# Optimization experiments

Measured on AMD Instinct MI355X. Metric: run time of the kernel, lower is better.

The kernel has to match this reference:

```python
import math
import jax, jax.numpy as jnp
import numpy as np

NUM_BUCKETS = 32
MAX_DISTANCE = 128
N_HEADS = 16
D_KV = 64


def _relative_position_bucket(relative_position, num_buckets=NUM_BUCKETS, max_distance=MAX_DISTANCE):
    # bidirectional variant (encoder): half the buckets for each sign
    nb = num_buckets // 2
    n = -relative_position
    ret = (n < 0).astype(jnp.int32) * nb
    n = jnp.abs(n)
    max_exact = nb // 2
    is_small = n < max_exact
    val_if_large = max_exact + (
        jnp.log(jnp.maximum(n, 1).astype(jnp.float32) / max_exact)
        / math.log(max_distance / max_exact)
        * (nb - max_exact)
    ).astype(jnp.int32)
    val_if_large = jnp.minimum(val_if_large, nb - 1)
    return ret + jnp.where(is_small, n, val_if_large)


def setup_inputs() -> dict:
    key = jax.random.key(0)
    ks = jax.random.split(key, 6)
    d_model = 1024
    inner = N_HEADS * D_KV
    scale = 1.0 / math.sqrt(d_model)
    x = jax.random.normal(ks[0], (2, 2048, d_model), dtype=jnp.float32)
    wq = jax.random.normal(ks[1], (d_model, inner), dtype=jnp.float32) * scale
    wk = jax.random.normal(ks[2], (d_model, inner), dtype=jnp.float32) * scale
    wv = jax.random.normal(ks[3], (d_model, inner), dtype=jnp.float32) * scale
    wo = jax.random.normal(ks[4], (inner, d_model), dtype=jnp.float32) * scale
    rel_emb = jax.random.normal(ks[5], (NUM_BUCKETS, N_HEADS), dtype=jnp.float32)
    return {"x": x, "wq": wq, "wk": wk, "wv": wv, "wo": wo, "rel_emb": rel_emb}


def reference(x, wq, wk, wv, wo, rel_emb):
    B, S, D = x.shape
    # QKV projections (no bias, T5 style), split heads -> [B, S, H, Dk]
    q = (x @ wq).reshape(B, S, N_HEADS, D_KV)
    k = (x @ wk).reshape(B, S, N_HEADS, D_KV)
    v = (x @ wv).reshape(B, S, N_HEADS, D_KV)
    # NOTE: T5 does NOT scale by 1/sqrt(d_kv)
    scores = jnp.einsum("bqhd,bkhd->bhqk", q, k)  # [B, H, S, S]
    # relative position bias
    ctx = jnp.arange(S)[:, None]
    mem = jnp.arange(S)[None, :]
    buckets = _relative_position_bucket(mem - ctx)  # [S, S]
    bias = rel_emb[buckets]  # [S, S, H]
    bias = jnp.transpose(bias, (2, 0, 1))[None]  # [1, H, S, S]
    scores = scores + bias
    weights = jax.nn.softmax(scores.astype(jnp.float32), axis=-1).astype(scores.dtype)
    context = jnp.einsum("bhqk,bkhd->bqhd", weights, v).reshape(B, S, N_HEADS * D_KV)
    return context @ wo
```

## Files before the change

### kernel.cpp

```cpp
#include <hip/hip_runtime.h>
#include <hip/hip_bf16.h>

typedef __attribute__((ext_vector_type(8))) _Float16 f16x8;
typedef __attribute__((ext_vector_type(4))) float f32x4;
typedef unsigned short u16;
typedef unsigned int u32;

#define S_LEN 2048
#define NH    16
#define DK    64
#define DMODEL 1024
#define LOG2E 1.44269504f
#define NTILES (S_LEN / 64)

union F16U { _Float16 h; u16 u; };
__device__ __forceinline__ u16 f2h(float f) {
    F16U v; v.h = (_Float16)f; return v.u;
}

__device__ __forceinline__ void gl16(const u16* g, u16* l) {
    __builtin_amdgcn_global_load_lds(
        (__attribute__((address_space(1))) void*)(u16*)g,
        (__attribute__((address_space(3))) void*)l, 16, 0, 0);
}

__global__ __launch_bounds__(256) void prep_kernel(
    const float* __restrict__ X,
    const float* __restrict__ Wq, const float* __restrict__ Wk,
    const float* __restrict__ Wv, const float* __restrict__ Wo,
    const float* __restrict__ rel_emb,
    u16* __restrict__ Xf, u16* __restrict__ WT, float* __restrict__ tab)
{
    __shared__ __align__(16) float T[64 * 68];
    const int bid = blockIdx.x;
    const int tid = threadIdx.x;

    if (bid < 2048) {
        long i8 = ((long)bid * 256 + tid) * 8;
        float4 a = *(const float4*)&X[i8];
        float4 b = *(const float4*)&X[i8 + 4];
        *(ushort4*)&Xf[i8] =
            make_ushort4(f2h(a.x), f2h(a.y), f2h(a.z), f2h(a.w));
        *(ushort4*)&Xf[i8 + 4] =
            make_ushort4(f2h(b.x), f2h(b.y), f2h(b.z), f2h(b.w));
    } else if (bid < 3072) {
        const int w0 = bid - 2048;
        const int z = w0 >> 8, rem = w0 & 255;
        const int k0 = (rem >> 4) * 64, n0 = (rem & 15) * 64;
        const float* src = (z == 0) ? Wq : (z == 1) ? Wk
                         : (z == 2) ? Wv : Wo;
        u16* dT = WT + (long)z * 1048576;
        #pragma unroll
        for (int u = 0; u < 4; u++) {
            int w = tid + u * 256;
            int r = w >> 4, c4 = (w & 15) * 4;
            *(float4*)&T[r * 68 + c4] =
                *(const float4*)&src[(long)(k0 + r) * DMODEL + n0 + c4];
        }
        __syncthreads();
        #pragma unroll
        for (int u = 0; u < 4; u++) {
            int w = tid + u * 256;
            int n = w >> 4, kc = (w & 15) * 4;
            *(ushort4*)&dT[(long)(n0 + n) * DMODEL + k0 + kc] = make_ushort4(
                f2h(T[(kc + 0) * 68 + n]), f2h(T[(kc + 1) * 68 + n]),
                f2h(T[(kc + 2) * 68 + n]), f2h(T[(kc + 3) * 68 + n]));
        }
    } else {
        int idx = (bid - 3072) * 256 + tid;
        int h = idx >> 12;
        int t = idx & 4095;
        int rp = t - 2048;
        int n = -rp;
        int ret = 0;
        if (n < 0) { ret = 16; n = -n; }
        int inner;
        if (n < 8) {
            inner = n;
        } else {
            inner = 8 + (n >= 12) + (n >= 16) + (n >= 23) + (n >= 32)
                      + (n >= 46) + (n >= 64) + (n >= 91);
            if (inner > 15) inner = 15;
        }
        tab[h * 4096 + t] = rel_emb[(ret + inner) * NH + h] * LOG2E;
    }
}

__global__ __launch_bounds__(256, 3) void gemm_qkv_mfma(
    const u16* __restrict__ Xf, const u16* __restrict__ WT,
    u16* __restrict__ Qf, u16* __restrict__ Kf, u16* __restrict__ VT)
{
    const int z = blockIdx.z;
    const u16* BT = WT + (long)z * 1048576;

    __shared__ __align__(16) u16 Ah[128 * 64], Bh[128 * 64];

    const int tid = threadIdx.x;
    const int wv = tid >> 6, lane = tid & 63;
    const int g = lane >> 4, li = lane & 15;
    const int wr = wv >> 1, wc = wv & 1;
    const int bm = blockIdx.y * 128, bn = blockIdx.x * 128;

    const int sr = lane >> 3;
    const int sb = ((lane & 7) ^ sr) * 8;
    const u16* Asrc[4]; const u16* Bsrc[4];
    u16* Adst[4]; u16* Bdst[4];
    #pragma unroll
    for (int u = 0; u < 4; u++) {
        const int c = wv * 4 + u;
        const int row = c * 8 + sr;
        Asrc[u] = &Xf[(long)(bm + row) * DMODEL + sb];
        Bsrc[u] = &BT[(long)(bn + row) * DMODEL + sb];
        Adst[u] = &Ah[c * 512];
        Bdst[u] = &Bh[c * 512];
    }

    int roA[4][2], roB[4][2];
    #pragma unroll
    for (int i = 0; i < 4; i++)
        #pragma unroll
        for (int ks = 0; ks < 2; ks++) {
            int RA = wr * 64 + i * 16 + li;
            int RB = wc * 64 + i * 16 + li;
            roA[i][ks] = RA * 64 + (((ks * 4 + g) ^ (li & 7)) * 8);
            roB[i][ks] = RB * 64 + (((ks * 4 + g) ^ (li & 7)) * 8);
        }

    f32x4 acc[4][4];
    #pragma unroll
    for (int i = 0; i < 4; i++)
        #pragma unroll
        for (int j = 0; j < 4; j++) acc[i][j] = (f32x4){0.f, 0.f, 0.f, 0.f};

    for (int k0 = 0; k0 < DMODEL; k0 += 64) {
        #pragma unroll
        for (int u = 0; u < 4; u++) {
            gl16(Asrc[u] + k0, Adst[u]);
            gl16(Bsrc[u] + k0, Bdst[u]);
        }
        __syncthreads();

        #pragma unroll
        for (int ks = 0; ks < 2; ks++) {
            f16x8 a_h[4], b_h[4];
            #pragma unroll
            for (int i = 0; i < 4; i++) a_h[i] = *(const f16x8*)&Ah[roA[i][ks]];
            #pragma unroll
            for (int j = 0; j < 4; j++) b_h[j] = *(const f16x8*)&Bh[roB[j][ks]];
            #pragma unroll
            for (int i = 0; i < 4; i++)
                #pragma unroll
                for (int j = 0; j < 4; j++)
                    acc[i][j] = __builtin_amdgcn_mfma_f32_16x16x32_f16(
                        a_h[i], b_h[j], acc[i][j], 0, 0, 0);
        }
        __syncthreads();
    }

    if (z == 2) {
        #pragma unroll
        for (int i = 0; i < 4; i++) {
            int s_base = bm + wr * 64 + i * 16 + g * 4;
            int bb = s_base >> 11, s = s_base & 2047;
            #pragma unroll
            for (int j = 0; j < 4; j++) {
                int gcol = bn + wc * 64 + j * 16 + li;
                int hh = gcol >> 6, d = gcol & 63;
                long idx = (((long)(bb * NH + hh)) * DK + d) * S_LEN + s;
                *(ushort4*)&VT[idx] = make_ushort4(
                    f2h(acc[i][j][0]), f2h(acc[i][j][1]),
                    f2h(acc[i][j][2]), f2h(acc[i][j][3]));
            }
        }
    } else {
        u16* O = (z == 0) ? Qf : Kf;
        #pragma unroll
        for (int i = 0; i < 4; i++) {
            #pragma unroll
            for (int r = 0; r < 4; r++) {
                int grow = bm + wr * 64 + i * 16 + g * 4 + r;
                int bb = grow >> 11, s = grow & 2047;
                #pragma unroll
                for (int j = 0; j < 4; j++) {
                    int gcol = bn + wc * 64 + j * 16 + li;
                    int hh = gcol >> 6, d = gcol & 63;
                    long idx = (((long)(bb * NH + hh)) * S_LEN + s) * DK + d;
                    O[idx] = f2h(acc[i][j][r]);
                }
            }
        }
    }
}

__global__ __launch_bounds__(256, 3) void gemm_out_mfma(
    const u16* __restrict__ Ab, const u16* __restrict__ WT,
    float* __restrict__ O)
{
    const u16* BT = WT + 3L * 1048576;
    __shared__ __align__(16) u16 Ah[128 * 64], Bh[128 * 64];

    const int tid = threadIdx.x;
    const int wv = tid >> 6, lane = tid & 63;
    const int g = lane >> 4, li = lane & 15;
    const int wr = wv >> 1, wc = wv & 1;
    const int bm = blockIdx.y * 128, bn = blockIdx.x * 128;

    const int sr = lane >> 3;
    const int sb = ((lane & 7) ^ sr) * 8;
    const u16* Asrc[4]; const u16* Bsrc[4];
    u16* Adst[4]; u16* Bdst[4];
    #pragma unroll
    for (int u = 0; u < 4; u++) {
        const int c = wv * 4 + u;
        const int row = c * 8 + sr;
        Asrc[u] = &Ab[(long)(bm + row) * DMODEL + sb];
        Bsrc[u] = &BT[(long)(bn + row) * DMODEL + sb];
        Adst[u] = &Ah[c * 512];
        Bdst[u] = &Bh[c * 512];
    }

    int roA[4][2], roB[4][2];
    #pragma unroll
    for (int i = 0; i < 4; i++)
        #pragma unroll
        for (int ks = 0; ks < 2; ks++) {
            int RA = wr * 64 + i * 16 + li;
            int RB = wc * 64 + i * 16 + li;
            roA[i][ks] = RA * 64 + (((ks * 4 + g) ^ (li & 7)) * 8);
            roB[i][ks] = RB * 64 + (((ks * 4 + g) ^ (li & 7)) * 8);
        }

    f32x4 acc[4][4];
    #pragma unroll
    for (int i = 0; i < 4; i++)
        #pragma unroll
        for (int j = 0; j < 4; j++) acc[i][j] = (f32x4){0.f, 0.f, 0.f, 0.f};

    for (int k0 = 0; k0 < DMODEL; k0 += 64) {
        #pragma unroll
        for (int u = 0; u < 4; u++) {
            gl16(Asrc[u] + k0, Adst[u]);
            gl16(Bsrc[u] + k0, Bdst[u]);
        }
        __syncthreads();

        #pragma unroll
        for (int ks = 0; ks < 2; ks++) {
            f16x8 a_h[4], b_h[4];
            #pragma unroll
            for (int i = 0; i < 4; i++) a_h[i] = *(const f16x8*)&Ah[roA[i][ks]];
            #pragma unroll
            for (int j = 0; j < 4; j++) b_h[j] = *(const f16x8*)&Bh[roB[j][ks]];
            #pragma unroll
            for (int i = 0; i < 4; i++)
                #pragma unroll
                for (int j = 0; j < 4; j++)
                    acc[i][j] = __builtin_amdgcn_mfma_f32_16x16x32_f16(
                        a_h[i], b_h[j], acc[i][j], 0, 0, 0);
        }
        __syncthreads();
    }

    #pragma unroll
    for (int i = 0; i < 4; i++)
        #pragma unroll
        for (int r = 0; r < 4; r++) {
            int grow = bm + wr * 64 + i * 16 + g * 4 + r;
            #pragma unroll
            for (int j = 0; j < 4; j++) {
                int gcol = bn + wc * 64 + j * 16 + li;
                O[(long)grow * DMODEL + gcol] = acc[i][j][r];
            }
        }
}

__global__ __launch_bounds__(256, 4) void attn_mfma(
    const u16* __restrict__ Qf, const u16* __restrict__ Kf,
    const u16* __restrict__ VT, const float* __restrict__ tab,
    u16* __restrict__ ctxb)
{
    __shared__ __align__(16) u16 Ks[2][4096];
    __shared__ __align__(16) u16 Vs[2][4096];

    const int tid = threadIdx.x;
    const int wv = tid >> 6, lane = tid & 63;
    const int g = lane >> 4, li = lane & 15;

    const int nbid = (blockIdx.x & 7) * 128 + (blockIdx.x >> 3);
    const int qblk = nbid & 31;
    const int h = (nbid >> 5) & 15;
    const int b = nbid >> 9;
    const int q0 = qblk * 64;
    const long bh = b * NH + h;
    const int qloc = wv * 16 + li;

    const u16* KhG = Kf + bh * (S_LEN * DK);
    const u16* VtG = VT + bh * (DK * S_LEN);
    const float* th0 = tab + h * 4096;
    const float* thq = th0 + 2048 - q0 - qloc + g * 4;

    const int sr  = lane >> 3;
    const int sd8 = ((lane & 7) ^ sr) * 8;
    const int c0 = wv * 2, c1 = wv * 2 + 1;
    const u16* Kg0 = KhG + (long)(c0 * 8 + sr) * DK + sd8;
    const u16* Kg1 = KhG + (long)(c1 * 8 + sr) * DK + sd8;
    const u16* Vg0 = VtG + (long)(c0 * 8 + sr) * S_LEN + sd8;
    const u16* Vg1 = VtG + (long)(c1 * 8 + sr) * S_LEN + sd8;

    const int sw  = (li & 7) * 8;
    const int roA = (g * 8) ^ sw;
    const int roB = (g * 8 + 32) ^ sw;
    const int rrow = li * 64;

    f16x8 q0f, q1f;
    {
        long qrow = bh * S_LEN + q0 + qloc;
        const u16* ph = Qf + qrow * DK + g * 8;
        q0f = *(const f16x8*)ph;  q1f = *(const f16x8*)(ph + 32);
    }
    const float bias_hi = th0[2048 + 512];
    const float bias_lo = th0[2048 - 512];

    gl16(Kg0, &Ks[0][c0 * 512]);
    gl16(Kg1, &Ks[0][c1 * 512]);
    gl16(Vg0, &Vs[0][c0 * 512]);
    gl16(Vg1, &Vs[0][c1 * 512]);
    __syncthreads();

    f32x4 Oc[4];
    #pragma unroll
    for (int n = 0; n < 4; n++) Oc[n] = (f32x4){0.f, 0.f, 0.f, 0.f};
    float mP = -1e30f, lR = 0.f;

    int cur = 0;
    for (int t = 0; t < NTILES; ++t) {
        const int kt0 = t * 64;

        if (t + 1 < NTILES) {
            const long ko = (long)(kt0 + 64) * DK;
            gl16(Kg0 + ko, &Ks[cur ^ 1][c0 * 512]);
            gl16(Kg1 + ko, &Ks[cur ^ 1][c1 * 512]);
            gl16(Vg0 + kt0 + 64, &Vs[cur ^ 1][c0 * 512]);
            gl16(Vg1 + kt0 + 64, &Vs[cur ^ 1][c1 * 512]);
        }

        float bia[4][4];
        const int dd = kt0 - q0;
        if (dd >= 192 || dd <= -192) {
            const float bc = (dd > 0) ? bias_hi : bias_lo;
            #pragma unroll
            for (int m = 0; m < 4; m++)
                #pragma unroll
                for (int r = 0; r < 4; r++) bia[m][r] = bc;
        } else {
            const float* tb = thq + kt0;
            #pragma unroll
            for (int m = 0; m < 4; m++)
                #pragma unroll
                for (int r = 0; r < 4; r++) bia[m][r] = tb[m * 16 + r];
        }

        f32x4 Sa[4];
        __builtin_amdgcn_s_setprio(1);
        #pragma unroll
        for (int m = 0; m < 4; m++) {
            const u16* kp = &Ks[cur][m * 1024 + rrow];
            f16x8 k0 = *(const f16x8*)(kp + roA);
            f16x8 k1 = *(const f16x8*)(kp + roB);
            f32x4 s = (f32x4){0.f, 0.f, 0.f, 0.f};
            s = __builtin_amdgcn_mfma_f32_16x16x32_f16(k0, q0f, s, 0, 0, 0);
            s = __builtin_amdgcn_mfma_f32_16x16x32_f16(k1, q1f, s, 0, 0, 0);
            Sa[m] = s;
        }
        __builtin_amdgcn_s_setprio(0);

        #pragma unroll
        for (int m = 0; m < 4; m++)
            #pragma unroll
            for (int r = 0; r < 4; r++)
                Sa[m][r] = fmaf(Sa[m][r], LOG2E, bia[m][r]);

        float mm[4];
        #pragma unroll
        for (int m = 0; m < 4; m++)
            mm[m] = fmaxf(fmaxf(Sa[m][0], Sa[m][1]),
                          fmaxf(Sa[m][2], Sa[m][3]));
        float pm = fmaxf(fmaxf(mm[0], mm[1]), fmaxf(mm[2], mm[3]));
        pm = fmaxf(pm, __shfl_xor(pm, 16));
        pm = fmaxf(pm, __shfl_xor(pm, 32));

        if (__any(pm > mP)) {
            float mn = fmaxf(mP, pm);
            float alpha = __builtin_amdgcn_exp2f(mP - mn);
            mP = mn;
            lR *= alpha;
            float aO[4];
            #pragma unroll
            for (int r = 0; r < 4; r++) aO[r] = __shfl(alpha, g * 4 + r);
            #pragma unroll
            for (int n = 0; n < 4; n++)
                #pragma unroll
                for (int r = 0; r < 4; r++) Oc[n][r] *= aO[r];
        }

        float sm[4];
        #pragma unroll
        for (int m = 0; m < 4; m++) {
            #pragma unroll
            for (int r = 0; r < 4; r++)
                Sa[m][r] = __builtin_amdgcn_exp2f(Sa[m][r] - mP);
            sm[m] = (Sa[m][0] + Sa[m][1]) + (Sa[m][2] + Sa[m][3]);
        }
        float ls = (sm[0] + sm[1]) + (sm[2] + sm[3]);
        ls += __shfl_xor(ls, 16);
        ls += __shfl_xor(ls, 32);
        lR += ls;

        u32 y0, y1, y2, y3, y4, y5, y6, y7;
        {
            y0 = f2h(Sa[0][0]) | ((u32)f2h(Sa[0][1]) << 16);
            y1 = f2h(Sa[0][2]) | ((u32)f2h(Sa[0][3]) << 16);
            y2 = f2h(Sa[1][0]) | ((u32)f2h(Sa[1][1]) << 16);
            y3 = f2h(Sa[1][2]) | ((u32)f2h(Sa[1][3]) << 16);
            y4 = f2h(Sa[2][0]) | ((u32)f2h(Sa[2][1]) << 16);
            y5 = f2h(Sa[2][2]) | ((u32)f2h(Sa[2][3]) << 16);
            y6 = f2h(Sa[3][0]) | ((u32)f2h(Sa[3][1]) << 16);
            y7 = f2h(Sa[3][2]) | ((u32)f2h(Sa[3][3]) << 16);
        }
        {
            bool hi = (lane & 32) != 0;
            u32 s0 = hi ? y0 : y2, s1 = hi ? y1 : y3;
            u32 s4 = hi ? y4 : y6, s5 = hi ? y5 : y7;
            u32 r0 = __shfl_xor((int)s0, 32);
            u32 r1 = __shfl_xor((int)s1, 32);
            u32 r4 = __shfl_xor((int)s4, 32);
            u32 r5 = __shfl_xor((int)s5, 32);
            if (hi) { y0 = r0; y1 = r1; y4 = r4; y5 = r5; }
            else    { y2 = r0; y3 = r1; y6 = r4; y7 = r5; }
        }
        {
            bool hi = (lane & 16) != 0;
            u32 s0 = hi ? y0 : y2, s1 = hi ? y1 : y3;
            u32 s4 = hi ? y4 : y6, s5 = hi ? y5 : y7;
            u32 r0 = __shfl_xor((int)s0, 16);
            u32 r1 = __shfl_xor((int)s1, 16);
            u32 r4 = __shfl_xor((int)s4, 16);
            u32 r5 = __shfl_xor((int)s5, 16);
            if (hi) { y0 = r0; y1 = r1; y4 = r4; y5 = r5; }
            else    { y2 = r0; y3 = r1; y6 = r4; y7 = r5; }
        }
        union { uint4 u; f16x8 h; } P0, P1;
        P0.u = make_uint4(y0, y1, y2, y3);
        P1.u = make_uint4(y4, y5, y6, y7);

        __builtin_amdgcn_s_setprio(1);
        #pragma unroll
        for (int n = 0; n < 4; n++) {
            const u16* vp = &Vs[cur][n * 1024 + rrow];
            f16x8 v0 = *(const f16x8*)(vp + roA);
            f16x8 v1 = *(const f16x8*)(vp + roB);
            Oc[n] = __builtin_amdgcn_mfma_f32_16x16x32_f16(P0.h, v0, Oc[n], 0, 0, 0);
            Oc[n] = __builtin_amdgcn_mfma_f32_16x16x32_f16(P1.h, v1, Oc[n], 0, 0, 0);
        }
        __builtin_amdgcn_s_setprio(0);

        __syncthreads();
        cur ^= 1;
    }

    float linv = 1.0f / lR;
    float iv[4];
    #pragma unroll
    for (int r = 0; r < 4; r++) iv[r] = __shfl(linv, g * 4 + r);
    #pragma unroll
    for (int n = 0; n < 4; n++)
        #pragma unroll
        for (int r = 0; r < 4; r++)
            ctxb[((long)(b * S_LEN + q0 + wv * 16 + g * 4 + r)) * DMODEL
                 + h * DK + n * 16 + li] = f2h(Oc[n][r] * iv[r]);
}

extern "C" void kernel_launch(void* const* d_in, const int* in_sizes, int n_in,
                              void* d_out, int out_size, void* d_ws, size_t ws_size,
                              hipStream_t stream)
{
    const float* x    = (const float*)d_in[0];
    const float* wq   = (const float*)d_in[1];
    const float* wk   = (const float*)d_in[2];
    const float* wv   = (const float*)d_in[3];
    const float* wo   = (const float*)d_in[4];
    const float* rel  = (const float*)d_in[5];

    u16* W0 = (u16*)d_ws;
    u16* Xf  = W0;
    u16* Qf  = W0 + 4194304;
    u16* Kf  = W0 + 8388608;
    u16* VT  = W0 + 12582912;
    u16* WT  = W0 + 16777216;
    float* tab = (float*)(W0 + 20971520);
    u16* ctxb = Xf;

    prep_kernel<<<dim3(3328), dim3(256), 0, stream>>>(
        x, wq, wk, wv, wo, rel, Xf, WT, tab);
    gemm_qkv_mfma<<<dim3(8, 32, 3), dim3(256), 0, stream>>>(Xf, WT, Qf, Kf, VT);
    attn_mfma<<<dim3(1024), dim3(256), 0, stream>>>(Qf, Kf, VT, tab, ctxb);
    gemm_out_mfma<<<dim3(8, 32), dim3(256), 0, stream>>>(ctxb, WT, (float*)d_out);
}
```

Measured before the change: 203.9 us.

## Double-buffer GEMM LDS tiles with BK=32 and use packed f16 conversion in attention

Both projection GEMMs now use two LDS buffers with 32-wide K tiles, prefetching the next tile via global_load_lds while MFMAs run on the current one. This drops one barrier per iteration and overlaps global loads with compute, with a new XOR swizzle for the 32-column layout. The attention kernel also switches the probability packing to cvt_pkrtz, which rounds toward zero instead of to nearest and slightly changes numerics.

New measurement: 208.7 us. 1.02x slower.

```diff
diff --git a/kernel.cpp b/kernel.cpp
--- a/kernel.cpp
+++ b/kernel.cpp
@@ -16,6 +16,13 @@
 union F16U { _Float16 h; u16 u; };
 __device__ __forceinline__ u16 f2h(float f) {
     F16U v; v.h = (_Float16)f; return v.u;
+}
+
+__device__ __forceinline__ u32 pk2(float a, float b) {
+    typedef __attribute__((ext_vector_type(2))) __fp16 fp16x2;
+    union { fp16x2 h; u32 u; } v;
+    v.h = __builtin_amdgcn_cvt_pkrtz(a, b);
+    return v.u;
 }
 
 __device__ __forceinline__ void gl16(const u16* g, u16* l) {
@@ -93,7 +100,7 @@
     const int z = blockIdx.z;
     const u16* BT = WT + (long)z * 1048576;
 
-    __shared__ __align__(16) u16 Ah[128 * 64], Bh[128 * 64];
+    __shared__ __align__(16) u16 Ah[2][128 * 32], Bh[2][128 * 32];
 
     const int tid = threadIdx.x;
     const int wv = tid >> 6, lane = tid & 63;
@@ -101,60 +108,59 @@
     const int wr = wv >> 1, wc = wv & 1;
     const int bm = blockIdx.y * 128, bn = blockIdx.x * 128;
 
-    const int sr = lane >> 3;
-    const int sb = ((lane & 7) ^ sr) * 8;
-    const u16* Asrc[4]; const u16* Bsrc[4];
-    u16* Adst[4]; u16* Bdst[4];
-    #pragma unroll
-    for (int u = 0; u < 4; u++) {
-        const int c = wv * 4 + u;
-        const int row = c * 8 + sr;
-        Asrc[u] = &Xf[(long)(bm + row) * DMODEL + sb];
-        Bsrc[u] = &BT[(long)(bn + row) * DMODEL + sb];
-        Adst[u] = &Ah[c * 512];
-        Bdst[u] = &Bh[c * 512];
-    }
-
-    int roA[4][2], roB[4][2];
+    const int srr = lane >> 2;
+    const int sb32 = ((lane & 3) ^ ((lane >> 3) & 3)) * 8;
+    const int c0 = wv * 2, c1 = wv * 2 + 1;
+    const u16* Ag0 = &Xf[(long)(bm + c0 * 16 + srr) * DMODEL + sb32];
+    const u16* Ag1 = &Xf[(long)(bm + c1 * 16 + srr) * DMODEL + sb32];
+    const u16* Bg0 = &BT[(long)(bn + c0 * 16 + srr) * DMODEL + sb32];
+    const u16* Bg1 = &BT[(long)(bn + c1 * 16 + srr) * DMODEL + sb32];
+
+    const int rsw = (li >> 1) & 3;
+    const int rko = ((g ^ rsw) * 8);
+    int roA[4], roB[4];
+    #pragma unroll
+    for (int i = 0; i < 4; i++) {
+        roA[i] = (wr * 64 + i * 16 + li) * 32 + rko;
+        roB[i] = (wc * 64 + i * 16 + li) * 32 + rko;
+    }
+
+    f32x4 acc[4][4];
     #pragma unroll
     for (int i = 0; i < 4; i++)
         #pragma unroll
-        for (int ks = 0; ks < 2; ks++) {
-            int RA = wr * 64 + i * 16 + li;
-            int RB = wc * 64 + i * 16 + li;
-            roA[i][ks] = RA * 64 + (((ks * 4 + g) ^ (li & 7)) * 8);
-            roB[i][ks] = RB * 64 + (((ks * 4 + g) ^ (li & 7)) * 8);
-        }
-
-    f32x4 acc[4][4];
-    #pragma unroll
-    for (int i = 0; i < 4; i++)
-        #pragma unroll
         for (int j = 0; j < 4; j++) acc[i][j] = (f32x4){0.f, 0.f, 0.f, 0.f};
 
-    for (int k0 = 0; k0 < DMODEL; k0 += 64) {
-        #pragma unroll
-        for (int u = 0; u < 4; u++) {
-            gl16(Asrc[u] + k0, Adst[u]);
-            gl16(Bsrc[u] + k0, Bdst[u]);
-        }
+    gl16(Ag0, &Ah[0][c0 * 512]);
+    gl16(Ag1, &Ah[0][c1 * 512]);
+    gl16(Bg0, &Bh[0][c0 * 512]);
+    gl16(Bg1, &Bh[0][c1 * 512]);
+    __syncthreads();
+
+    int cur = 0;
+    for (int t = 0; t < 32; ++t) {
+        if (t + 1 < 32) {
+            const int k0 = (t + 1) * 32;
+            gl16(Ag0 + k0, &Ah[cur ^ 1][c0 * 512]);
+            gl16(Ag1 + k0, &Ah[cur ^ 1][c1 * 512]);
+            gl16(Bg0 + k0, &Bh[cur ^ 1][c0 * 512]);
+            gl16(Bg1 + k0, &Bh[cur ^ 1][c1 * 512]);
+        }
+
+        f16x8 a_h[4], b_h[4];
+        #pragma unroll
+        for (int i = 0; i < 4; i++) a_h[i] = *(const f16x8*)&Ah[cur][roA[i]];
+        #pragma unroll
+        for (int j = 0; j < 4; j++) b_h[j] = *(const f16x8*)&Bh[cur][roB[j]];
+        #pragma unroll
+        for (int i = 0; i < 4; i++)
+            #pragma unroll
+            for (int j = 0; j < 4; j++)
+                acc[i][j] = __builtin_amdgcn_mfma_f32_16x16x32_f16(
+                    a_h[i], b_h[j], acc[i][j], 0, 0, 0);
+
         __syncthreads();
-
-        #pragma unroll
-        for (int ks = 0; ks < 2; ks++) {
-            f16x8 a_h[4], b_h[4];
-            #pragma unroll
-            for (int i = 0; i < 4; i++) a_h[i] = *(const f16x8*)&Ah[roA[i][ks]];
-            #pragma unroll
-            for (int j = 0; j < 4; j++) b_h[j] = *(const f16x8*)&Bh[roB[j][ks]];
-            #pragma unroll
-            for (int i = 0; i < 4; i++)
-                #pragma unroll
-                for (int j = 0; j < 4; j++)
-                    acc[i][j] = __builtin_amdgcn_mfma_f32_16x16x32_f16(
-                        a_h[i], b_h[j], acc[i][j], 0, 0, 0);
-        }
-        __syncthreads();
+        cur ^= 1;
     }
 
     if (z == 2) {
@@ -197,7 +203,7 @@
     float* __restrict__ O)
 {
     const u16* BT = WT + 3L * 1048576;
-    __shared__ __align__(16) u16 Ah[128 * 64], Bh[128 * 64];
+    __shared__ __align__(16) u16 Ah[2][128 * 32], Bh[2][128 * 32];
 
     const int tid = threadIdx.x;
     const int wv = tid >> 6, lane = tid & 63;
@@ -205,60 +211,59 @@
     const int wr = wv >> 1, wc = wv & 1;
     const int bm = blockIdx.y * 128, bn = blockIdx.x * 128;
 
-    const int sr = lane >> 3;
-    const int sb = ((lane & 7) ^ sr) * 8;
-    const u16* Asrc[4]; const u16* Bsrc[4];
-    u16* Adst[4]; u16* Bdst[4];
-    #pragma unroll
-    for (int u = 0; u < 4; u++) {
-        const int c = wv * 4 + u;
-        const int row = c * 8 + sr;
-        Asrc[u] = &Ab[(long)(bm + row) * DMODEL + sb];
-        Bsrc[u] = &BT[(long)(bn + row) * DMODEL + sb];
-        Adst[u] = &Ah[c * 512];
-        Bdst[u] = &Bh[c * 512];
-    }
-
-    int roA[4][2], roB[4][2];
+    const int srr = lane >> 2;
+    const int sb32 = ((lane & 3) ^ ((lane >> 3) & 3)) * 8;
+    const int c0 = wv * 2, c1 = wv * 2 + 1;
+    const u16* Ag0 = &Ab[(long)(bm + c0 * 16 + srr) * DMODEL + sb32];
+    const u16* Ag1 = &Ab[(long)(bm + c1 * 16 + srr) * DMODEL + sb32];
+    const u16* Bg0 = &BT[(long)(bn + c0 * 16 + srr) * DMODEL + sb32];
+    const u16* Bg1 = &BT[(long)(bn + c1 * 16 + srr) * DMODEL + sb32];
+
+    const int rsw = (li >> 1) & 3;
+    const int rko = ((g ^ rsw) * 8);
+    int roA[4], roB[4];
+    #pragma unroll
+    for (int i = 0; i < 4; i++) {
+        roA[i] = (wr * 64 + i * 16 + li) * 32 + rko;
+        roB[i] = (wc * 64 + i * 16 + li) * 32 + rko;
+    }
+
+    f32x4 acc[4][4];
     #pragma unroll
     for (int i = 0; i < 4; i++)
         #pragma unroll
-        for (int ks = 0; ks < 2; ks++) {
-            int RA = wr * 64 + i * 16 + li;
-            int RB = wc * 64 + i * 16 + li;
-            roA[i][ks] = RA * 64 + (((ks * 4 + g) ^ (li & 7)) * 8);
-            roB[i][ks] = RB * 64 + (((ks * 4 + g) ^ (li & 7)) * 8);
-        }
-
-    f32x4 acc[4][4];
-    #pragma unroll
-    for (int i = 0; i < 4; i++)
-        #pragma unroll
         for (int j = 0; j < 4; j++) acc[i][j] = (f32x4){0.f, 0.f, 0.f, 0.f};
 
-    for (int k0 = 0; k0 < DMODEL; k0 += 64) {
-        #pragma unroll
-        for (int u = 0; u < 4; u++) {
-            gl16(Asrc[u] + k0, Adst[u]);
-            gl16(Bsrc[u] + k0, Bdst[u]);
-        }
+    gl16(Ag0, &Ah[0][c0 * 512]);
+    gl16(Ag1, &Ah[0][c1 * 512]);
+    gl16(Bg0, &Bh[0][c0 * 512]);
+    gl16(Bg1, &Bh[0][c1 * 512]);
+    __syncthreads();
+
+    int cur = 0;
+    for (int t = 0; t < 32; ++t) {
+        if (t + 1 < 32) {
+            const int k0 = (t + 1) * 32;
+            gl16(Ag0 + k0, &Ah[cur ^ 1][c0 * 512]);
+            gl16(Ag1 + k0, &Ah[cur ^ 1][c1 * 512]);
+            gl16(Bg0 + k0, &Bh[cur ^ 1][c0 * 512]);
+            gl16(Bg1 + k0, &Bh[cur ^ 1][c1 * 512]);
+        }
+
+        f16x8 a_h[4], b_h[4];
+        #pragma unroll
+        for (int i = 0; i < 4; i++) a_h[i] = *(const f16x8*)&Ah[cur][roA[i]];
+        #pragma unroll
+        for (int j = 0; j < 4; j++) b_h[j] = *(const f16x8*)&Bh[cur][roB[j]];
+        #pragma unroll
+        for (int i = 0; i < 4; i++)
+            #pragma unroll
+            for (int j = 0; j < 4; j++)
+                acc[i][j] = __builtin_amdgcn_mfma_f32_16x16x32_f16(
+                    a_h[i], b_h[j], acc[i][j], 0, 0, 0);
+
         __syncthreads();
-
-        #pragma unroll
-        for (int ks = 0; ks < 2; ks++) {
-            f16x8 a_h[4], b_h[4];
-            #pragma unroll
-            for (int i = 0; i < 4; i++) a_h[i] = *(const f16x8*)&Ah[roA[i][ks]];
-            #pragma unroll
-            for (int j = 0; j < 4; j++) b_h[j] = *(const f16x8*)&Bh[roB[j][ks]];
-            #pragma unroll
-            for (int i = 0; i < 4; i++)
-                #pragma unroll
-                for (int j = 0; j < 4; j++)
-                    acc[i][j] = __builtin_amdgcn_mfma_f32_16x16x32_f16(
-                        a_h[i], b_h[j], acc[i][j], 0, 0, 0);
-        }
-        __syncthreads();
+        cur ^= 1;
     }
 
     #pragma unroll
@@ -418,14 +423,14 @@
 
         u32 y0, y1, y2, y3, y4, y5, y6, y7;
         {
-            y0 = f2h(Sa[0][0]) | ((u32)f2h(Sa[0][1]) << 16);
-            y1 = f2h(Sa[0][2]) | ((u32)f2h(Sa[0][3]) << 16);
-            y2 = f2h(Sa[1][0]) | ((u32)f2h(Sa[1][1]) << 16);
-            y3 = f2h(Sa[1][2]) | ((u32)f2h(Sa[1][3]) << 16);
-            y4 = f2h(Sa[2][0]) | ((u32)f2h(Sa[2][1]) << 16);
-            y5 = f2h(Sa[2][2]) | ((u32)f2h(Sa[2][3]) << 16);
-            y6 = f2h(Sa[3][0]) | ((u32)f2h(Sa[3][1]) << 16);
-            y7 = f2h(Sa[3][2]) | ((u32)f2h(Sa[3][3]) << 16);
+            y0 = pk2(Sa[0][0], Sa[0][1]);
+            y1 = pk2(Sa[0][2], Sa[0][3]);
+            y2 = pk2(Sa[1][0], Sa[1][1]);
+            y3 = pk2(Sa[1][2], Sa[1][3]);
+            y4 = pk2(Sa[2][0], Sa[2][1]);
+            y5 = pk2(Sa[2][2], Sa[2][3]);
+            y6 = pk2(Sa[3][0], Sa[3][1]);
+            y7 = pk2(Sa[3][2], Sa[3][3]);
         }
         {
             bool hi = (lane & 32) != 0;
```
